# Kernel tuning notes

Measured on AMD Instinct MI355X. Metric: run time of the kernel, lower is better.

The kernel has to match this reference:

```python
import jax, jax.numpy as jnp
import numpy as np

H = 8          # num_heads
FOCUS = 3      # focusing_factor
EPS = 1e-6


def _disagreement(h):
    # h: [B, Hn, N, d]; mean of pairwise cosine-sim matrix with diagonal zeroed
    B, Hn, N, d = h.shape
    hn = h / jnp.maximum(jnp.linalg.norm(h, axis=-1, keepdims=True), 1e-12)
    sim_sum = jnp.sum(jnp.einsum('bhnd,bhmd->bhnm', hn, hn))
    diag_sum = jnp.sum(hn * hn)  # diagonal entries of the sim matrix
    return (sim_sum - diag_sum) / (B * Hn * N * N)


def setup_inputs() -> dict:
    key = jax.random.key(0)
    ks = jax.random.split(key, 10)
    B, N, C, K = 4, 1024, 512, 10
    s = 0.02
    return {
        'Q': jax.random.normal(ks[0], (B, N, C), jnp.float32),
        'adj_mat': jax.random.randint(ks[1], (B, N, K), 0, N),
        'Wq': jax.random.normal(ks[2], (C, C), jnp.float32) * s,
        'bq': jnp.zeros((C,), jnp.float32),
        'Wk': jax.random.normal(ks[3], (C, C), jnp.float32) * s,
        'bk': jnp.zeros((C,), jnp.float32),
        'Wv': jax.random.normal(ks[4], (C, C), jnp.float32) * s,
        'bv': jnp.zeros((C,), jnp.float32),
        'scale_p': jnp.zeros((1, 1, C), jnp.float32),  # torch init: zeros
        'Wconv': jax.random.normal(ks[5], (C, C, K + 1), jnp.float32) * s,
        'bconv': jnp.zeros((C,), jnp.float32),
        'W2': jax.random.normal(ks[6], (C, C), jnp.float32) * s,
        'b2': jnp.zeros((C,), jnp.float32),
        'ln_g': jnp.ones((C,), jnp.float32),
        'ln_b': jnp.zeros((C,), jnp.float32),
        'Wo': jax.random.normal(ks[7], (C, C), jnp.float32) * s,
        'bo': jnp.zeros((C,), jnp.float32),
    }


def _forward(Q, adj_mat, Wq, bq, Wk, bk, Wv, bv, scale_p, Wconv, bconv,
             W2, b2, ln_g, ln_b, Wo, bo):
    B, N, C = Q.shape
    d = C // H
    q = Q @ Wq + bq
    k = Q @ Wk + bk
    v = Q @ Wv + bv

    # LocalFeatureExtractor on v: gather K neighbors, conv over (channel, K+1) window
    neigh = v[jnp.arange(B)[:, None, None], adj_mat]          # [B,N,K,C]
    feats = jnp.concatenate([v[:, :, None, :], neigh], axis=2)  # [B,N,K+1,C]
    conv = jnp.einsum('bntc,oct->bno', feats, Wconv) + bconv   # full-window conv1d
    x_local = conv @ W2 + b2                                   # [B,N,C]

    # kernelized q/k with softplus scale and focused normalization
    q = jax.nn.relu(q) + EPS
    k = jax.nn.relu(k) + EPS
    scale = jax.nn.softplus(scale_p)
    q = q / scale
    k = k / scale

    def focus(x):
        n = jnp.linalg.norm(x, axis=-1, keepdims=True)
        return (x / (n + EPS)) ** FOCUS * n

    q = focus(q)
    k = focus(k)

    q = q.reshape(B, N, H, d).transpose(0, 2, 1, 3)
    k = k.reshape(B, N, H, d).transpose(0, 2, 1, 3)
    vh = v.reshape(B, N, H, d).transpose(0, 2, 1, 3)

    # linear attention: z normalization and kv summarization
    z = 1.0 / (jnp.einsum('bhnd,bhd->bhn', q, k.mean(axis=2)) + EPS)  # [B,H,N]
    kv = jnp.einsum('bhnd,bhne->bhde', k, vh) / N                     # [B,H,d,d]
    x = jnp.einsum('bhnd,bhde->bhne', q, kv) * z[..., None]           # [B,H,N,d]

    loss_local = _disagreement(vh)
    loss_kv = _disagreement(kv)

    x = x.transpose(0, 2, 1, 3).reshape(B, N, C) + x_local
    x4 = x.reshape(B, H, N, d)  # raw memory reinterpretation, matches torch .reshape
    loss_out = _disagreement(x4)
    loss = (loss_local + loss_out + loss_kv) / 3.0
    x = x4.reshape(B, N, C)

    # out_proj: LayerNorm then Linear
    mu = x.mean(axis=-1, keepdims=True)
    var = jnp.mean((x - mu) ** 2, axis=-1, keepdims=True)
    xn = (x - mu) / jnp.sqrt(var + 1e-5) * ln_g + ln_b
    out = xn @ Wo + bo
    return out, loss


def reference(Q, adj_mat, Wq, bq, Wk, bk, Wv, bv, scale_p, Wconv, bconv,
              W2, b2, ln_g, ln_b, Wo, bo):
    return _forward(Q, adj_mat, Wq, bq, Wk, bk, Wv, bv, scale_p, Wconv, bconv,
                    W2, b2, ln_g, ln_b, Wo, bo)
```

## Files before the change

### kernel.cpp

```cpp
#include <hip/hip_runtime.h>
#include <math.h>

#define TOK_TOTAL 4096
#define KNB 10
#define MATE 2097152

typedef __attribute__((ext_vector_type(8))) short short8;
typedef __attribute__((ext_vector_type(4))) float floatx4;
typedef unsigned short ushort;

__device__ __forceinline__ floatx4 mfma16(short8 a, short8 b, floatx4 c) {
  return __builtin_amdgcn_mfma_f32_16x16x32_bf16(a, b, c, 0, 0, 0);
}

__device__ __forceinline__ ushort f2bf(float f) {
  union { float f; unsigned int u; } x; x.f = f;
  unsigned int r = x.u + 0x7fffu + ((x.u >> 16) & 1u);
  return (ushort)(r >> 16);
}

__device__ __forceinline__ float bf2f(ushort u) {
  union { unsigned int u; float f; } x; x.u = ((unsigned int)u) << 16;
  return x.f;
}

__device__ __forceinline__ float lane_bcast(float v, int l) {
  union { float f; int i; } x; x.f = v;
  x.i = __builtin_amdgcn_readlane(x.i, l);
  return x.f;
}

__device__ __forceinline__ void glds16(const ushort* g, ushort* l) {
  __builtin_amdgcn_global_load_lds((const __attribute__((address_space(1))) void*)g,
                                   (__attribute__((address_space(3))) void*)l, 16, 0, 0);
}

__device__ __forceinline__ float wave_reduce_sum(float v) {
#pragma unroll
  for (int m = 32; m >= 1; m >>= 1) v += __shfl_xor(v, m, 64);
  return v;
}

__device__ __forceinline__ float block_reduce_sum_256(float v, float* red) {
  v = wave_reduce_sum(v);
  __syncthreads();
  if ((threadIdx.x & 63) == 0) red[threadIdx.x >> 6] = v;
  __syncthreads();
  return red[0] + red[1] + red[2] + red[3];
}

__global__ __launch_bounds__(256) void prep_kernel(const float* __restrict__ Wq,
                                                   const float* __restrict__ Wk,
                                                   const float* __restrict__ Wv,
                                                   const float* __restrict__ W2p,
                                                   const float* __restrict__ Wo,
                                                   const float* __restrict__ Wconv,
                                                   const float* __restrict__ Q,
                                                   const float* __restrict__ bq,
                                                   const float* __restrict__ bk,
                                                   const float* __restrict__ bv,
                                                   ushort* __restrict__ WT,
                                                   ushort* __restrict__ BcY,
                                                   float* __restrict__ biasqkv,
                                                   ushort* __restrict__ Qb,
                                                   float* __restrict__ zbase,
                                                   float* __restrict__ loss) {
  int blk = blockIdx.x;
  if (blk < 1280) {
    __shared__ float tile[32][33];
    int zz = blk >> 8, rem = blk & 255;
    const float* W = (zz == 0) ? Wq : (zz == 1) ? Wk : (zz == 2) ? Wv
                     : (zz == 3) ? W2p : Wo;
    ushort* Wt = WT + (size_t)zz * 262144;
    int n0 = (rem & 15) * 32, k0 = (rem >> 4) * 32;
    int tx = threadIdx.x & 31, ty = threadIdx.x >> 5;
#pragma unroll
    for (int i = 0; i < 32; i += 8)
      tile[ty + i][tx] = W[(size_t)(k0 + ty + i) * 512 + n0 + tx];
    __syncthreads();
#pragma unroll
    for (int i = 0; i < 32; i += 8)
      Wt[(size_t)(n0 + ty + i) * 512 + k0 + tx] = f2bf(tile[tx][ty + i]);
  } else if (blk < 2304) {
    int i = (blk - 1280) * 256 + threadIdx.x;
    const float* src = Wconv + (size_t)i * 11;
    int o = i >> 9, c = i & 511;
#pragma unroll
    for (int t = 0; t < 11; ++t)
      BcY[(((size_t)(t * 512 + o)) << 9) + c] = f2bf(src[t]);
  } else if (blk == 2304) {
    for (int i = threadIdx.x; i < 1536; i += 256)
      biasqkv[i] = (i < 512) ? bq[i] : ((i < 1024) ? bk[i - 512] : bv[i - 1024]);
  } else if (blk < 4353) {
    int i = (blk - 2305) * 256 + threadIdx.x;
    float4 v = *(const float4*)(Q + (size_t)i * 4);
    Qb[(size_t)i * 4 + 0] = f2bf(v.x);
    Qb[(size_t)i * 4 + 1] = f2bf(v.y);
    Qb[(size_t)i * 4 + 2] = f2bf(v.z);
    Qb[(size_t)i * 4 + 3] = f2bf(v.w);
  } else {
    int i = (blk - 4353) * 256 + threadIdx.x;
    if (i < 34840) {
      float4 z; z.x = 0.f; z.y = 0.f; z.z = 0.f; z.w = 0.f;
      ((float4*)zbase)[i] = z;
    }
    if (blk == 4353 && threadIdx.x == 0) loss[0] = 0.f;
  }
}

__global__ __launch_bounds__(256, 3) void gemm128(const ushort* __restrict__ A,
                                                  const ushort* __restrict__ Bt,
                                                  ushort* __restrict__ Cb,
                                                  int Ktot, int Ncols) {
  __shared__ __align__(16) ushort As[3][4096];
  __shared__ __align__(16) ushort Bs[3][4096];
  int tid = threadIdx.x, w = tid >> 6, lane = tid & 63;
  int lm = lane & 15, kq = lane >> 4;
  int row0 = blockIdx.y * 128, col0 = blockIdx.x * 128;
  int wm = w >> 1, wn = w & 1;

  bool isA = (w < 2);
  const ushort* gs[4];
  int go[4];
#pragma unroll
  for (int i = 0; i < 4; ++i) {
    int slab = (w & 1) * 4 + i;
    const ushort* base = isA ? (A + (size_t)(row0 + slab * 16 + lm) * Ktot)
                             : (Bt + (size_t)(col0 + slab * 16 + lm) * Ktot);
    gs[i] = base + kq * 8;
    go[i] = slab * 512;
  }

  floatx4 acc[4][4];
#pragma unroll
  for (int i = 0; i < 4; ++i)
#pragma unroll
    for (int j = 0; j < 4; ++j)
#pragma unroll
      for (int e = 0; e < 4; ++e) acc[i][j][e] = 0.f;

#pragma unroll
  for (int i = 0; i < 4; ++i) glds16(gs[i], (isA ? As[0] : Bs[0]) + go[i]);
#pragma unroll
  for (int i = 0; i < 4; ++i) glds16(gs[i] + 32, (isA ? As[1] : Bs[1]) + go[i]);
  asm volatile("s_waitcnt vmcnt(4)" ::: "memory");
  __builtin_amdgcn_s_barrier();

  int nsteps = Ktot >> 5;
  for (int s = 0; s < nsteps; ++s) {
    int cur = s % 3;
    if (s + 2 < nsteps) {
      int nb = (s + 2) % 3;
      ushort* dst = (isA ? As[nb] : Bs[nb]);
      int koff = (s + 2) << 5;
#pragma unroll
      for (int i = 0; i < 4; ++i) glds16(gs[i] + koff, dst + go[i]);
    }
    const ushort* Acur = As[cur];
    const ushort* Bcur = Bs[cur];
    short8 a[4], b[4];
#pragma unroll
    for (int mt = 0; mt < 4; ++mt)
      a[mt] = *(const short8*)(&Acur[(wm * 4 + mt) * 512 + lane * 8]);
#pragma unroll
    for (int nt = 0; nt < 4; ++nt)
      b[nt] = *(const short8*)(&Bcur[(wn * 4 + nt) * 512 + lane * 8]);
#pragma unroll
    for (int mt = 0; mt < 4; ++mt)
#pragma unroll
      for (int nt = 0; nt < 4; ++nt)
        acc[mt][nt] = mfma16(a[mt], b[nt], acc[mt][nt]);
    if (s + 1 < nsteps) {
      if (s + 2 < nsteps) {
        asm volatile("s_waitcnt vmcnt(4)" ::: "memory");
      } else {
        asm volatile("s_waitcnt vmcnt(0)" ::: "memory");
      }
      __builtin_amdgcn_s_barrier();
    }
  }

#pragma unroll
  for (int mt = 0; mt < 4; ++mt) {
#pragma unroll
    for (int nt = 0; nt < 4; ++nt) {
      int col = col0 + wn * 64 + nt * 16 + lm;
#pragma unroll
      for (int r = 0; r < 4; ++r) {
        int row = row0 + wm * 64 + mt * 16 + kq * 4 + r;
        Cb[(size_t)row * Ncols + col] = f2bf(acc[mt][nt][r]);
      }
    }
  }
}

__global__ __launch_bounds__(256, 4) void gemm128_qkv(const ushort* __restrict__ A,
                                                      const ushort* __restrict__ Bt,
                                                      const float* __restrict__ bias,
                                                      float* __restrict__ outf,
                                                      ushort* __restrict__ vb) {
  __shared__ __align__(16) ushort As[2][4096];
  __shared__ __align__(16) ushort Bs[2][4096];
  int tid = threadIdx.x, w = tid >> 6, lane = tid & 63;
  int lm = lane & 15, kq = lane >> 4;
  int row0 = blockIdx.y * 128, col0 = blockIdx.x * 128;
  int wm = w >> 1, wn = w & 1;

  bool isA = (w < 2);
  const ushort* gs[4];
  int go[4];
#pragma unroll
  for (int i = 0; i < 4; ++i) {
    int slab = (w & 1) * 4 + i;
    const ushort* base = isA ? (A + (size_t)(row0 + slab * 16 + lm) * 512)
                             : (Bt + (size_t)(col0 + slab * 16 + lm) * 512);
    gs[i] = base + kq * 8;
    go[i] = slab * 512;
  }

  floatx4 acc[4][4];
#pragma unroll
  for (int i = 0; i < 4; ++i)
#pragma unroll
    for (int j = 0; j < 4; ++j)
#pragma unroll
      for (int e = 0; e < 4; ++e) acc[i][j][e] = 0.f;

#pragma unroll
  for (int i = 0; i < 4; ++i)
    glds16(gs[i], (isA ? As[0] : Bs[0]) + go[i]);

  for (int s = 0; s < 16; ++s) {
    int buf = s & 1;
    __syncthreads();
    if (s + 1 < 16) {
      int koff = (s + 1) << 5;
      ushort* dst = (isA ? As[buf ^ 1] : Bs[buf ^ 1]);
#pragma unroll
      for (int i = 0; i < 4; ++i) glds16(gs[i] + koff, dst + go[i]);
    }
    short8 a[4], b[4];
#pragma unroll
    for (int mt = 0; mt < 4; ++mt)
      a[mt] = *(const short8*)(&As[buf][(wm * 4 + mt) * 512 + lane * 8]);
#pragma unroll
    for (int nt = 0; nt < 4; ++nt)
      b[nt] = *(const short8*)(&Bs[buf][(wn * 4 + nt) * 512 + lane * 8]);
#pragma unroll
    for (int mt = 0; mt < 4; ++mt)
#pragma unroll
      for (int nt = 0; nt < 4; ++nt)
        acc[mt][nt] = mfma16(a[mt], b[nt], acc[mt][nt]);
  }

#pragma unroll
  for (int mt = 0; mt < 4; ++mt) {
#pragma unroll
    for (int nt = 0; nt < 4; ++nt) {
      int col = col0 + wn * 64 + nt * 16 + lm;
      int mat = col >> 9, cc = col & 511;
      float bs = bias[col];
#pragma unroll
      for (int r = 0; r < 4; ++r) {
        int row = row0 + wm * 64 + mt * 16 + kq * 4 + r;
        float val = acc[mt][nt][r] + bs;
        size_t idx = (size_t)row * 512 + cc;
        outf[(size_t)mat * MATE + idx] = val;
        if (mat == 2) vb[idx] = f2bf(val);
      }
    }
  }
}

__global__ __launch_bounds__(256) void gather_add_bias(const ushort* __restrict__ Y,
                                                       const int* __restrict__ adj,
                                                       const float* __restrict__ bias,
                                                       ushort* __restrict__ convb) {
  int n = (blockIdx.x << 1) + (threadIdx.x >> 7);
  int b10 = (n >> 10) << 10;
  int o = (threadIdx.x & 127) << 2;
  float4 bs = *(const float4*)(bias + o);
  float a0 = bs.x, a1 = bs.y, a2 = bs.z, a3 = bs.w;
#pragma unroll
  for (int t = 0; t < 11; ++t) {
    int src = (t == 0) ? n : (b10 + adj[(size_t)n * KNB + (t - 1)]);
    const ushort* p = Y + (size_t)src * 5632 + (size_t)t * 512 + o;
    uint2 u = *(const uint2*)p;
    a0 += bf2f((ushort)(u.x & 0xffff));
    a1 += bf2f((ushort)(u.x >> 16));
    a2 += bf2f((ushort)(u.y & 0xffff));
    a3 += bf2f((ushort)(u.y >> 16));
  }
  uint2 w;
  w.x = (unsigned)f2bf(a0) | ((unsigned)f2bf(a1) << 16);
  w.y = (unsigned)f2bf(a2) | ((unsigned)f2bf(a3) << 16);
  *(uint2*)(convb + (size_t)n * 512 + o) = w;
}

__global__ __launch_bounds__(256) void gather_add(const ushort* __restrict__ Y,
                                                  const int* __restrict__ adj,
                                                  float* __restrict__ convf,
                                                  int t0, int ntaps, int ncols) {
  int n = blockIdx.x;
  int b10 = (n >> 10) << 10;
  int o = threadIdx.x * 2;
  float a0 = 0.f, a1 = 0.f;
  for (int t = t0; t < t0 + ntaps; ++t) {
    int src = (t == 0) ? n : (b10 + adj[(size_t)n * KNB + (t - 1)]);
    const ushort* p = Y + (size_t)src * ncols + (size_t)(t - t0) * 512 + o;
    a0 += bf2f(p[0]);
    a1 += bf2f(p[1]);
  }
  convf[(size_t)n * 512 + o] += a0;
  convf[(size_t)n * 512 + o + 1] += a1;
}

__global__ __launch_bounds__(256) void convbias_cast(const float* __restrict__ cf,
                                                     const float* __restrict__ bias,
                                                     ushort* __restrict__ cb) {
  int i = blockIdx.x * 256 + threadIdx.x;
  float4 v = *(const float4*)(cf + (size_t)i * 4);
  int c = (i * 4) & 511;
  cb[(size_t)i * 4 + 0] = f2bf(v.x + bias[c + 0]);
  cb[(size_t)i * 4 + 1] = f2bf(v.y + bias[c + 1]);
  cb[(size_t)i * 4 + 2] = f2bf(v.z + bias[c + 2]);
  cb[(size_t)i * 4 + 3] = f2bf(v.w + bias[c + 3]);
}

__global__ __launch_bounds__(256) void gemm64(const ushort* __restrict__ A,
                                              const ushort* __restrict__ Bt,
                                              const float* __restrict__ bias,
                                              float* __restrict__ Cf,
                                              ushort* __restrict__ Cb,
                                              int Ktot) {
  __shared__ __align__(16) ushort As[2][4096];
  __shared__ __align__(16) ushort Bs[2][4096];
  int tid = threadIdx.x, w = tid >> 6, lane = tid & 63;
  int lm = lane & 15, kq = lane >> 4;
  int row0 = blockIdx.y * 64, col0 = blockIdx.x * 64;
  int wm = w >> 1, wn = w & 1;

  const ushort* gsrc[4];
  int goff[4];
  bool isA = (w < 2);
#pragma unroll
  for (int i = 0; i < 4; ++i) {
    int l = w * 4 + i, t, j;
    const ushort* base;
    if (l < 8) { t = l >> 1; j = l & 1; base = A + (size_t)(row0 + t * 16 + lm) * Ktot; }
    else { int lb = l - 8; t = lb >> 1; j = lb & 1; base = Bt + (size_t)(col0 + t * 16 + lm) * Ktot; }
    gsrc[i] = base + j * 32 + kq * 8;
    goff[i] = t * 1024 + j * 512;
  }

  floatx4 acc[2][2];
#pragma unroll
  for (int i = 0; i < 2; ++i)
#pragma unroll
    for (int j = 0; j < 2; ++j)
#pragma unroll
      for (int e = 0; e < 4; ++e) acc[i][j][e] = 0.f;

#pragma unroll
  for (int i = 0; i < 4; ++i)
    glds16(gsrc[i], (isA ? As[0] : Bs[0]) + goff[i]);

  int nsteps = Ktot >> 6;
  for (int s = 0; s < nsteps; ++s) {
    int buf = s & 1;
    __syncthreads();
    if (s + 1 < nsteps) {
      int koff = (s + 1) << 6;
      ushort* dst = (isA ? As[buf ^ 1] : Bs[buf ^ 1]);
#pragma unroll
      for (int i = 0; i < 4; ++i) glds16(gsrc[i] + koff, dst + goff[i]);
    }
#pragma unroll
    for (int j = 0; j < 2; ++j) {
      short8 a0 = *(const short8*)(&As[buf][(wm * 2 + 0) * 1024 + j * 512 + lane * 8]);
      short8 a1 = *(const short8*)(&As[buf][(wm * 2 + 1) * 1024 + j * 512 + lane * 8]);
      short8 b0 = *(const short8*)(&Bs[buf][(wn * 2 + 0) * 1024 + j * 512 + lane * 8]);
      short8 b1 = *(const short8*)(&Bs[buf][(wn * 2 + 1) * 1024 + j * 512 + lane * 8]);
      acc[0][0] = mfma16(a0, b0, acc[0][0]);
      acc[0][1] = mfma16(a0, b1, acc[0][1]);
      acc[1][0] = mfma16(a1, b0, acc[1][0]);
      acc[1][1] = mfma16(a1, b1, acc[1][1]);
    }
  }

  int colb = col0 + wn * 32;
  int rowb = row0 + wm * 32 + kq * 4;
#pragma unroll
  for (int mt = 0; mt < 2; ++mt) {
#pragma unroll
    for (int nt = 0; nt < 2; ++nt) {
      int col = colb + nt * 16 + lm;
      float bs = bias[col];
#pragma unroll
      for (int r = 0; r < 4; ++r) {
        int row = rowb + mt * 16 + r;
        float val = acc[mt][nt][r] + bs;
        size_t idx = (size_t)row * 512 + col;
        if (Cf) Cf[idx] = val;
        if (Cb) Cb[idx] = f2bf(val);
      }
    }
  }
}

__global__ __launch_bounds__(256) void focus_kernel(float* __restrict__ x,
                                                    const float* __restrict__ scale_p) {
  __shared__ float red[4];
  int row = blockIdx.x;
  float* p = x + (size_t)row * 512;
  int tid = threadIdx.x;
  float sp0 = scale_p[tid], sp1 = scale_p[tid + 256];
  float sc0 = sp0 > 20.f ? sp0 : log1pf(expf(sp0));
  float sc1 = sp1 > 20.f ? sp1 : log1pf(expf(sp1));
  float v0 = (fmaxf(p[tid], 0.f) + 1e-6f) / sc0;
  float v1 = (fmaxf(p[tid + 256], 0.f) + 1e-6f) / sc1;
  float tot = block_reduce_sum_256(v0 * v0 + v1 * v1, red);
  float n = sqrtf(tot);
  float np = n + 1e-6f;
  float f = n / (np * np * np);
  p[tid] = v0 * v0 * v0 * f;
  p[tid + 256] = v1 * v1 * v1 * f;
}

__global__ __launch_bounds__(256) void kv_kernel(const float* __restrict__ kf,
                                                 const float* __restrict__ v,
                                                 float* __restrict__ kv,
                                                 float* __restrict__ Sacc,
                                                 float* __restrict__ Dacc,
                                                 float* __restrict__ kmean) {
  __shared__ float Ks[16][64];
  __shared__ float Vs[16][64];
  __shared__ float Spart[64];
  __shared__ float Kpart[64];
  __shared__ float Dpart;
  int bh = blockIdx.x >> 3, chunk = blockIdx.x & 7;
  int b = bh >> 3, h = bh & 7;
  int tid = threadIdx.x;
  int lr = tid >> 4, lc = (tid & 15) << 2;
  int tx = tid & 15, ty = tid >> 4;
  if (tid < 64) { Spart[tid] = 0.f; Kpart[tid] = 0.f; }
  if (tid == 0) Dpart = 0.f;
  __syncthreads();
  const float* kbase = kf + (size_t)b * 524288 + h * 64 + (size_t)chunk * 128 * 512;
  const float* vbase = v + (size_t)b * 524288 + h * 64 + (size_t)chunk * 128 * 512;
  float acc[4][4] = {};
  float Sloc[4] = {0.f, 0.f, 0.f, 0.f};
  float Kloc[4] = {0.f, 0.f, 0.f, 0.f};
  float Dloc = 0.f;
  for (int n0 = 0; n0 < 128; n0 += 16) {
    float4 ke = *(const float4*)(kbase + (size_t)(n0 + lr) * 512 + lc);
    *(float4*)(&Ks[lr][lc]) = ke;
    Kloc[0] += ke.x; Kloc[1] += ke.y; Kloc[2] += ke.z; Kloc[3] += ke.w;
    float4 ve = *(const float4*)(vbase + (size_t)(n0 + lr) * 512 + lc);
    *(float4*)(&Vs[lr][lc]) = ve;
    __syncthreads();
    float sq = ve.x * ve.x + ve.y * ve.y + ve.z * ve.z + ve.w * ve.w;
#pragma unroll
    for (int m = 1; m < 16; m <<= 1) sq += __shfl_xor(sq, m, 64);
    float cn = fmaxf(sqrtf(sq), 1e-12f);
    Sloc[0] += ve.x / cn; Sloc[1] += ve.y / cn;
    Sloc[2] += ve.z / cn; Sloc[3] += ve.w / cn;
    if ((tid & 15) == 0) Dloc += sq / (cn * cn);
#pragma unroll
    for (int kk = 0; kk < 16; ++kk) {
      float a[4], bb[4];
#pragma unroll
      for (int i = 0; i < 4; ++i) a[i] = Ks[kk][ty * 4 + i];
#pragma unroll
      for (int j = 0; j < 4; ++j) bb[j] = Vs[kk][tx * 4 + j];
#pragma unroll
      for (int i = 0; i < 4; ++i)
#pragma unroll
        for (int j = 0; j < 4; ++j) acc[i][j] += a[i] * bb[j];
    }
    __syncthreads();
  }
#pragma unroll
  for (int i = 0; i < 4; ++i)
#pragma unroll
    for (int j = 0; j < 4; ++j)
      atomicAdd(&kv[(size_t)bh * 4096 + (ty * 4 + i) * 64 + tx * 4 + j],
                acc[i][j] * (1.f / 1024.f));
#pragma unroll
  for (int i = 0; i < 4; ++i) {
    atomicAdd(&Spart[lc + i], Sloc[i]);
    atomicAdd(&Kpart[lc + i], Kloc[i]);
  }
  if ((tid & 15) == 0) atomicAdd(&Dpart, Dloc);
  __syncthreads();
  if (tid < 64) {
    atomicAdd(&Sacc[bh * 64 + tid], Spart[tid]);
    atomicAdd(&kmean[b * 512 + h * 64 + tid], Kpart[tid] * (1.f / 1024.f));
  }
  if (tid == 64) atomicAdd(&Dacc[bh], Dpart);
}

__global__ __launch_bounds__(512, 4) void attn_ln_kernel(const float* __restrict__ qf,
                                                         const float* __restrict__ kvf,
                                                         const float* __restrict__ kmean,
                                                         const float* __restrict__ x_local,
                                                         const float* __restrict__ scale_p,
                                                         const float* __restrict__ g,
                                                         const float* __restrict__ bp,
                                                         ushort* __restrict__ xn,
                                                         float* __restrict__ Sacc,
                                                         float* __restrict__ Dacc,
                                                         float* __restrict__ Skv,
                                                         float* __restrict__ Dkv) {
  __shared__ __align__(16) ushort kvs[32768];
  __shared__ float red[16];
  __shared__ float Sl[8][64];
  __shared__ float Dl[8];
  int r0 = blockIdx.x << 3;
  int b = r0 >> 10;
  int c = threadIdx.x, wv = c >> 6, lane = c & 63;
  const float4* kvg = (const float4*)(kvf + (size_t)b * 32768);
#pragma unroll
  for (int i = 0; i < 16; ++i) {
    float4 kvv = kvg[c + i * 512];
    int o = (c + i * 512) << 2;
    kvs[o + 0] = f2bf(kvv.x); kvs[o + 1] = f2bf(kvv.y);
    kvs[o + 2] = f2bf(kvv.z); kvs[o + 3] = f2bf(kvv.w);
  }
  float kmr = kmean[b * 512 + c];
  float gr = g[c], bpr = bp[c];
  float sp = scale_p[c];
  float sc = sp > 20.f ? sp : log1pf(expf(sp));
  float scinv = 1.f / sc;
  __syncthreads();
  unsigned int kvr[32];
#pragma unroll
  for (int i = 0; i < 32; ++i) {
    unsigned int lo = kvs[wv * 4096 + (2 * i) * 64 + lane];
    unsigned int hi = kvs[wv * 4096 + (2 * i + 1) * 64 + lane];
    kvr[i] = lo | (hi << 16);
  }
  float Sreg = 0.f, Dreg = 0.f;
  for (int r = 0; r < 8; ++r) {
    int row = r0 + r;
    float qraw = qf[(size_t)row * 512 + c];
    float xl = x_local[(size_t)row * 512 + c];
    float v0 = (fmaxf(qraw, 0.f) + 1e-6f) * scinv;
    float l2 = wave_reduce_sum(v0 * v0);
    if (lane == 0) red[wv] = l2;
    __syncthreads();
    float nq2 = red[0] + red[1] + red[2] + red[3] + red[4] + red[5] + red[6] + red[7];
    __syncthreads();
    float nq = sqrtf(nq2);
    float npq = nq + 1e-6f;
    float qv = v0 * v0 * v0 * (nq / (npq * npq * npq));
    float zd = wave_reduce_sum(qv * kmr);
    float zz = 1.f / (zd + 1e-6f);
    float s = 0.f;
#pragma unroll
    for (int i = 0; i < 32; ++i) {
      union { unsigned int u; float f; } lo, hi;
      lo.u = kvr[i] << 16;
      hi.u = kvr[i] & 0xffff0000u;
      s += lane_bcast(qv, 2 * i) * lo.f;
      s += lane_bcast(qv, 2 * i + 1) * hi.f;
    }
    float xv = s * zz + xl;
    float s1 = wave_reduce_sum(xv);
    float s2 = wave_reduce_sum(xv * xv);
    if (lane == 0) { red[wv] = s1; red[8 + wv] = s2; }
    __syncthreads();
    float tsum = red[0] + red[1] + red[2] + red[3] + red[4] + red[5] + red[6] + red[7];
    float tsq = red[8] + red[9] + red[10] + red[11] + red[12] + red[13] + red[14] + red[15];
    __syncthreads();
    float mu = tsum * (1.f / 512.f);
    float var = tsq * (1.f / 512.f) - mu * mu;
    float inv = rsqrtf(fmaxf(var, 0.f) + 1e-5f);
    xn[(size_t)row * 512 + c] = f2bf((xv - mu) * inv * gr + bpr);
    float norm = fmaxf(sqrtf(s2), 1e-12f);
    Sreg += xv / norm;
    Dreg += s2 / (norm * norm);
  }
  Sl[wv][lane] = Sreg;
  if (lane == 0) Dl[wv] = Dreg;
  __syncthreads();
  int gx = b * 8 + ((r0 & 1023) >> 7);
  if (c < 64) {
    float ssum = 0.f;
#pragma unroll
    for (int ww = 0; ww < 8; ++ww) ssum += Sl[ww][c];
    atomicAdd(&Sacc[gx * 64 + c], ssum);
  } else if (c == 64) {
    float dsum = 0.f;
#pragma unroll
    for (int ww = 0; ww < 8; ++ww) dsum += Dl[ww];
    atomicAdd(&Dacc[gx], dsum);
  }
  if ((blockIdx.x & 127) == 0) {
    float S2 = 0.f, D2 = 0.f;
#pragma unroll
    for (int i = 0; i < 32; ++i) {
      union { unsigned int u; float f; } lo, hi;
      lo.u = kvr[i] << 16;
      hi.u = kvr[i] & 0xffff0000u;
      float sq = wave_reduce_sum(lo.f * lo.f);
      float nrm = fmaxf(sqrtf(sq), 1e-12f);
      float hn = lo.f / nrm;
      S2 += hn; D2 += hn * hn;
      sq = wave_reduce_sum(hi.f * hi.f);
      nrm = fmaxf(sqrtf(sq), 1e-12f);
      hn = hi.f / nrm;
      S2 += hn; D2 += hn * hn;
    }
    float dt = wave_reduce_sum(D2);
    atomicAdd(&Skv[(b * 8 + wv) * 64 + lane], S2);
    if (lane == 0) atomicAdd(&Dkv[b * 8 + wv], dt);
  }
}

__global__ __launch_bounds__(64) void disagree_final_all(const float* __restrict__ Sall,
                                                         const float* __restrict__ Dall,
                                                         float s0, float s1, float s2,
                                                         float* __restrict__ loss) {
  int set = blockIdx.x >> 5, gg = blockIdx.x & 31;
  int l = threadIdx.x;
  float sv = Sall[set * 2048 + gg * 64 + l];
  float sim = wave_reduce_sum(sv * sv);
  if (l == 0) {
    float scale = (set == 0) ? s0 : (set == 1) ? s1 : s2;
    atomicAdd(loss, (sim - Dall[set * 32 + gg]) * scale);
  }
}

extern "C" void kernel_launch(void* const* d_in, const int* in_sizes, int n_in,
                              void* d_out, int out_size, void* d_ws, size_t ws_size,
                              hipStream_t stream) {
  const float* Q       = (const float*)d_in[0];
  const int*   adj     = (const int*)d_in[1];
  const float* Wq      = (const float*)d_in[2];
  const float* bq      = (const float*)d_in[3];
  const float* Wk      = (const float*)d_in[4];
  const float* bk      = (const float*)d_in[5];
  const float* Wv      = (const float*)d_in[6];
  const float* bv      = (const float*)d_in[7];
  const float* scale_p = (const float*)d_in[8];
  const float* Wconv   = (const float*)d_in[9];
  const float* bconv   = (const float*)d_in[10];
  const float* W2      = (const float*)d_in[11];
  const float* b2      = (const float*)d_in[12];
  const float* ln_g    = (const float*)d_in[13];
  const float* ln_b    = (const float*)d_in[14];
  const float* Wo      = (const float*)d_in[15];
  const float* bo      = (const float*)d_in[16];

  float* out = (float*)d_out;
  float* loss_slot = out + MATE;

  float* ws = (float*)d_ws;
  float* q0      = ws;
  float* k0      = q0 + MATE;
  float* v       = k0 + MATE;
  float* x_local = v + MATE;
  float* convf   = x_local + MATE;
  ushort* Qb    = (ushort*)(convf + MATE);
  ushort* vb    = Qb + MATE;
  ushort* convb = vb + MATE;
  ushort* xnb   = convb + MATE;
  ushort* WqT   = xnb + MATE;
  ushort* W2T   = WqT + 3 * 262144;
  ushort* WoT   = W2T + 262144;
  ushort* BcY   = WoT + 262144;
  float* biasqkv = (float*)(BcY + 5632 * 512);
  float* kmean = biasqkv + 1536;
  float* kvbuf = kmean + 2048;
  float* Sv    = kvbuf + 131072;
  float* Skv   = Sv + 2048;
  float* Sx    = Skv + 2048;
  float* Dv    = Sx + 2048;
  float* Dkv   = Dv + 32;
  float* Dx    = Dkv + 32;
  float* ytail = Dx + 32;
  ushort* Ybf  = (ushort*)ytail;

  size_t used_floats = (size_t)(ytail - ws);
  size_t avail_floats = (ws_size / 4 > used_floats) ? (ws_size / 4 - used_floats) : 0;
  int TC = (int)(avail_floats / (MATE / 2));
  if (TC < 1) TC = 1;
  if (TC > 11) TC = 11;

  prep_kernel<<<4490, 256, 0, stream>>>(Wq, Wk, Wv, W2, Wo, Wconv, Q,
                                        bq, bk, bv, WqT, BcY, biasqkv, Qb,
                                        kmean, loss_slot);

  gemm128_qkv<<<dim3(12, 32), 256, 0, stream>>>(Qb, WqT, biasqkv, q0, vb);

  if (TC >= 11) {
    gemm128<<<dim3(44, 32), 256, 0, stream>>>(vb, BcY, Ybf, 512, 5632);
    gather_add_bias<<<2048, 256, 0, stream>>>(Ybf, adj, bconv, convb);
  } else {
    hipMemsetAsync(convf, 0, MATE * sizeof(float), stream);
    for (int t0 = 0; t0 < 11; t0 += TC) {
      int nt = (11 - t0 < TC) ? (11 - t0) : TC;
      int ncols = nt * 512;
      gemm128<<<dim3(ncols / 128, 32), 256, 0, stream>>>(
          vb, BcY + (size_t)(t0 * 512) * 512, Ybf, 512, ncols);
      gather_add<<<4096, 256, 0, stream>>>(Ybf, adj, convf, t0, nt, ncols);
    }
    convbias_cast<<<2048, 256, 0, stream>>>(convf, bconv, convb);
  }

  gemm64<<<dim3(8, 64), 256, 0, stream>>>(convb, W2T, b2, x_local, nullptr, 512);

  focus_kernel<<<TOK_TOTAL, 256, 0, stream>>>(k0, scale_p);

  kv_kernel<<<256, 256, 0, stream>>>(k0, v, kvbuf, Sv, Dv, kmean);

  attn_ln_kernel<<<512, 512, 0, stream>>>(q0, kvbuf, kmean, x_local, scale_p,
                                          ln_g, ln_b, xnb, Sx, Dx, Skv, Dkv);

  disagree_final_all<<<96, 64, 0, stream>>>(Sv, Dv,
                                            1.f / (33554432.f * 3.f),
                                            1.f / (131072.f * 3.f),
                                            1.f / (33554432.f * 3.f), loss_slot);

  gemm64<<<dim3(8, 64), 256, 0, stream>>>(xnb, WoT, bo, out, nullptr, 512);
}
```

Baseline: 288.1 us.

## Enlarge conv GEMM tile to 256x128 with 512 threads and double buffering

```diff
diff --git a/kernel.cpp b/kernel.cpp
--- a/kernel.cpp
+++ b/kernel.cpp
@@ -108,25 +108,24 @@
   }
 }
 
-__global__ __launch_bounds__(256, 3) void gemm128(const ushort* __restrict__ A,
-                                                  const ushort* __restrict__ Bt,
-                                                  ushort* __restrict__ Cb,
-                                                  int Ktot, int Ncols) {
-  __shared__ __align__(16) ushort As[3][4096];
-  __shared__ __align__(16) ushort Bs[3][4096];
+__global__ __launch_bounds__(512, 4) void gemm_conv(const ushort* __restrict__ A,
+                                                    const ushort* __restrict__ Bt,
+                                                    ushort* __restrict__ Cb,
+                                                    int Ktot, int Ncols) {
+  __shared__ __align__(16) ushort SS[2][12288];
   int tid = threadIdx.x, w = tid >> 6, lane = tid & 63;
   int lm = lane & 15, kq = lane >> 4;
-  int row0 = blockIdx.y * 128, col0 = blockIdx.x * 128;
+  int row0 = blockIdx.y * 256, col0 = blockIdx.x * 128;
   int wm = w >> 1, wn = w & 1;
 
-  bool isA = (w < 2);
-  const ushort* gs[4];
-  int go[4];
-#pragma unroll
-  for (int i = 0; i < 4; ++i) {
-    int slab = (w & 1) * 4 + i;
-    const ushort* base = isA ? (A + (size_t)(row0 + slab * 16 + lm) * Ktot)
-                             : (Bt + (size_t)(col0 + slab * 16 + lm) * Ktot);
+  const ushort* gs[3];
+  int go[3];
+#pragma unroll
+  for (int i = 0; i < 3; ++i) {
+    int slab = 3 * w + i;
+    const ushort* base = (slab < 16)
+        ? (A + (size_t)(row0 + slab * 16 + lm) * Ktot)
+        : (Bt + (size_t)(col0 + (slab - 16) * 16 + lm) * Ktot);
     gs[i] = base + kq * 8;
     go[i] = slab * 512;
   }
@@ -140,44 +139,30 @@
       for (int e = 0; e < 4; ++e) acc[i][j][e] = 0.f;
 
 #pragma unroll
-  for (int i = 0; i < 4; ++i) glds16(gs[i], (isA ? As[0] : Bs[0]) + go[i]);
-#pragma unroll
-  for (int i = 0; i < 4; ++i) glds16(gs[i] + 32, (isA ? As[1] : Bs[1]) + go[i]);
-  asm volatile("s_waitcnt vmcnt(4)" ::: "memory");
-  __builtin_amdgcn_s_barrier();
+  for (int i = 0; i < 3; ++i) glds16(gs[i], SS[0] + go[i]);
 
   int nsteps = Ktot >> 5;
   for (int s = 0; s < nsteps; ++s) {
-    int cur = s % 3;
-    if (s + 2 < nsteps) {
-      int nb = (s + 2) % 3;
-      ushort* dst = (isA ? As[nb] : Bs[nb]);
-      int koff = (s + 2) << 5;
-#pragma unroll
-      for (int i = 0; i < 4; ++i) glds16(gs[i] + koff, dst + go[i]);
-    }
-    const ushort* Acur = As[cur];
-    const ushort* Bcur = Bs[cur];
+    int buf = s & 1;
+    __syncthreads();
+    if (s + 1 < nsteps) {
+      int koff = (s + 1) << 5;
+      ushort* dst = SS[buf ^ 1];
+#pragma unroll
+      for (int i = 0; i < 3; ++i) glds16(gs[i] + koff, dst + go[i]);
+    }
     short8 a[4], b[4];
 #pragma unroll
     for (int mt = 0; mt < 4; ++mt)
-      a[mt] = *(const short8*)(&Acur[(wm * 4 + mt) * 512 + lane * 8]);
+      a[mt] = *(const short8*)(&SS[buf][(wm * 4 + mt) * 512 + lane * 8]);
 #pragma unroll
     for (int nt = 0; nt < 4; ++nt)
-      b[nt] = *(const short8*)(&Bcur[(wn * 4 + nt) * 512 + lane * 8]);
+      b[nt] = *(const short8*)(&SS[buf][8192 + (wn * 4 + nt) * 512 + lane * 8]);
 #pragma unroll
     for (int mt = 0; mt < 4; ++mt)
 #pragma unroll
       for (int nt = 0; nt < 4; ++nt)
         acc[mt][nt] = mfma16(a[mt], b[nt], acc[mt][nt]);
-    if (s + 1 < nsteps) {
-      if (s + 2 < nsteps) {
-        asm volatile("s_waitcnt vmcnt(4)" ::: "memory");
-      } else {
-        asm volatile("s_waitcnt vmcnt(0)" ::: "memory");
-      }
-      __builtin_amdgcn_s_barrier();
-    }
   }
 
 #pragma unroll
@@ -695,14 +680,14 @@
   gemm128_qkv<<<dim3(12, 32), 256, 0, stream>>>(Qb, WqT, biasqkv, q0, vb);
 
   if (TC >= 11) {
-    gemm128<<<dim3(44, 32), 256, 0, stream>>>(vb, BcY, Ybf, 512, 5632);
+    gemm_conv<<<dim3(44, 16), 512, 0, stream>>>(vb, BcY, Ybf, 512, 5632);
     gather_add_bias<<<2048, 256, 0, stream>>>(Ybf, adj, bconv, convb);
   } else {
     hipMemsetAsync(convf, 0, MATE * sizeof(float), stream);
     for (int t0 = 0; t0 < 11; t0 += TC) {
       int nt = (11 - t0 < TC) ? (11 - t0) : TC;
       int ncols = nt * 512;
-      gemm128<<<dim3(ncols / 128, 32), 256, 0, stream>>>(
+      gemm_conv<<<dim3(ncols / 128, 16), 512, 0, stream>>>(
           vb, BcY + (size_t)(t0 * 512) * 512, Ybf, 512, ncols);
       gather_add<<<4096, 256, 0, stream>>>(Ybf, adj, convf, t0, nt, ncols);
     }
```

Measured after the change: 285.8 us. About the same (-0.8%).
